# Kernel tuning notes

Hardware: AMD Instinct MI355X
Metric: run time of the kernel (lower is better)

Reference implementation:

```python
import jax, jax.numpy as jnp
import numpy as np

B, S, D_MODEL, D_ATTN = 4, 4096, 2048, 2048


def setup_inputs() -> dict:
    key = jax.random.key(0)
    ks = jax.random.split(key, 6)
    s = 0.02
    return {
        "x": jax.random.normal(ks[0], (B, S, D_MODEL), dtype=jnp.float32),
        "Wq": jax.random.normal(ks[1], (D_ATTN, D_MODEL), dtype=jnp.float32) * s,
        "Wk": jax.random.normal(ks[2], (D_ATTN, D_MODEL), dtype=jnp.float32) * s,
        "Wv": jax.random.normal(ks[3], (D_ATTN, D_MODEL), dtype=jnp.float32) * s,
        "Wo": jax.random.normal(ks[4], (D_MODEL, D_ATTN), dtype=jnp.float32) * s,
        "bo": jnp.zeros((D_MODEL,), dtype=jnp.float32),
    }


def reference(x, Wq, Wk, Wv, Wo, bo):
    # q,k,v: [B,S,d_attn] via bias-free linears (torch Linear: x @ W.T)
    q = jnp.einsum('bsd,ad->bsa', x, Wq)
    k = jnp.einsum('bsd,ad->bsa', x, Wk)
    v = jnp.einsum('bsd,ad->bsa', x, Wv)
    # logits: [B,S,S]; NOTE: source scales by sqrt(d_model), not d_attn
    scale = 1.0 / jnp.sqrt(jnp.asarray(x.shape[-1], dtype=x.dtype))
    logits = jnp.einsum('bqa,bka->bqk', q, k) * scale
    attn = jax.nn.softmax(logits, axis=-1)
    attn_out = jnp.einsum('bqk,bka->bqa', attn, v)
    return jnp.einsum('bqa,da->bqd', attn_out, Wo) + bo
```

## Files before the change

kernel.cpp:

```cpp
#include <hip/hip_runtime.h>
#include <hip/hip_bf16.h>


#define S_ 4096
#define DM_ 2048
#define DA_ 2048
#define NB_ 4

typedef __attribute__((ext_vector_type(8))) short short8;
typedef __attribute__((ext_vector_type(4))) float f32x4;
typedef __attribute__((ext_vector_type(8))) unsigned short ushort8;

__device__ __forceinline__ void gload_lds16(const void* g, void* l) {
  __builtin_amdgcn_global_load_lds(
      (const __attribute__((address_space(1))) void*)g,
      (__attribute__((address_space(3))) void*)l, 16, 0, 0);
}

__device__ __forceinline__ unsigned short f2bf(float f) {
  __hip_bfloat16 h = __float2bfloat16(f);
  return __builtin_bit_cast(unsigned short, h);
}

#define STAGE_A(par, h, kt)                                                    \
  {                                                                            \
    const __hip_bfloat16* s0 = Asrc + (size_t)((h)*128) * lda + (kt)*64;       \
    gload_lds16(s0, dstA + (par)*32768 + (h)*16384);                           \
    gload_lds16(s0 + (size_t)64 * lda, dstA + (par)*32768 + (h)*16384 + 8192); \
  }
#define STAGE_B(par, h, kt)                                                    \
  {                                                                            \
    const __hip_bfloat16* s0 = Bsrc + (size_t)((h)*128) * ldb + (kt)*64;       \
    gload_lds16(s0, dstB + (par)*32768 + (h)*16384);                           \
    gload_lds16(s0 + (size_t)64 * ldb, dstB + (par)*32768 + (h)*16384 + 8192); \
  }
#define LDA_FRAG(par, mi, i, kk) \
  (*(const short8*)(ldsAr + (par)*32768 + ((mi)*2 + (i)) * 2048 + (kk)*1024))
#define LDB_FRAG(par, j, kk) \
  (*(const short8*)(ldsBr + (par)*32768 + (j)*2048 + (kk)*1024))

#define MFMA_ON(mi, AF)                                                     \
  __builtin_amdgcn_s_setprio(1);                                            \
  _Pragma("unroll") for (int i = 0; i < 2; ++i)                             \
      _Pragma("unroll") for (int j = 0; j < 4; ++j)                         \
          _Pragma("unroll") for (int kk = 0; kk < 2; ++kk)                  \
              acc[(mi)*2 + i][j] = __builtin_amdgcn_mfma_f32_16x16x32_bf16( \
                  AF[i][kk], Bf[j][kk], acc[(mi)*2 + i][j], 0, 0, 0);       \
  __builtin_amdgcn_s_setprio(0);

#define PHASE_SYNC_PRE                               \
  __builtin_amdgcn_s_barrier();                      \
  asm volatile("s_waitcnt lgkmcnt(0)" ::: "memory"); \
  __builtin_amdgcn_sched_barrier(0);

template <int PAR>
__device__ __forceinline__ void tile_body(
    int t, int NT, const __hip_bfloat16* __restrict__ Asrc,
    const __hip_bfloat16* __restrict__ Bsrc, int lda, int ldb, char* dstA,
    char* dstB, const char* ldsAr, const char* ldsBr, f32x4 (&acc)[8][4]) {
  const int tn = min(t + 1, NT - 1);
  const int tf = min(t + 2, NT - 1);
  short8 Bf[4][2], Af[2][2];

#pragma unroll
  for (int j = 0; j < 4; ++j)
#pragma unroll
    for (int kk = 0; kk < 2; ++kk) Bf[j][kk] = LDB_FRAG(PAR, j, kk);
#pragma unroll
  for (int i = 0; i < 2; ++i)
#pragma unroll
    for (int kk = 0; kk < 2; ++kk) Af[i][kk] = LDA_FRAG(PAR, 0, i, kk);
  STAGE_A(PAR ^ 1, 0, tn);
  PHASE_SYNC_PRE
  MFMA_ON(0, Af)
  __builtin_amdgcn_s_barrier();

#pragma unroll
  for (int i = 0; i < 2; ++i)
#pragma unroll
    for (int kk = 0; kk < 2; ++kk) Af[i][kk] = LDA_FRAG(PAR, 1, i, kk);
  STAGE_A(PAR ^ 1, 1, tn);
  PHASE_SYNC_PRE
  MFMA_ON(1, Af)
  __builtin_amdgcn_s_barrier();

#pragma unroll
  for (int i = 0; i < 2; ++i)
#pragma unroll
    for (int kk = 0; kk < 2; ++kk) Af[i][kk] = LDA_FRAG(PAR, 2, i, kk);
  STAGE_B(PAR, 0, tf);
  PHASE_SYNC_PRE
  MFMA_ON(2, Af)
  __builtin_amdgcn_s_barrier();

#pragma unroll
  for (int i = 0; i < 2; ++i)
#pragma unroll
    for (int kk = 0; kk < 2; ++kk) Af[i][kk] = LDA_FRAG(PAR, 3, i, kk);
  STAGE_B(PAR, 1, tf);
  PHASE_SYNC_PRE
  MFMA_ON(3, Af)
  asm volatile("s_waitcnt vmcnt(4)" ::: "memory");
  __builtin_amdgcn_s_barrier();
  __builtin_amdgcn_sched_barrier(0);
}

template <int EPI>
__device__ __forceinline__ void gemm8_body(
    int wgin, int nwg, const __hip_bfloat16* __restrict__ A,
    const __hip_bfloat16* __restrict__ Bm, void* __restrict__ Cv,
    const float* __restrict__ bias, float* __restrict__ aux, int N, int K,
    int lda, int ldb, int ldc, float scale, long strideA, long strideB,
    long strideC) {
  __shared__ alignas(16) char lds[131072];
  const int tid = threadIdx.x;
  const int lane = tid & 63;
  const int w = tid >> 6;
  const int wr = w >> 2, wc = w & 3;

  int wg = (wgin & 7) * (nwg >> 3) + (wgin >> 3);
  const int nbn = N >> 8;
  const int nstx = nbn >> 2;
  const int st = wg >> 4;
  const int bm = (st / nstx) * 4 + ((wg >> 2) & 3);
  const int bn = (st % nstx) * 4 + (wg & 3);

  A += (long)blockIdx.y * strideA;
  Bm += (long)blockIdx.y * strideB;

  const int R = ((w >> 1) << 4) + (lane >> 2);
  const int Cc = ((w & 1) << 5) + (((lane & 3) << 3) ^ ((lane & 32) >> 1));
  const __hip_bfloat16* Asrc = A + (size_t)(bm * 256 + R) * lda + Cc;
  const __hip_bfloat16* Bsrc = Bm + (size_t)(bn * 256 + R) * ldb + Cc;
  char* dstA = lds + w * 1024 + lane * 16;
  char* dstB = dstA + 65536;

  const int fr = lane & 15;
  const int fk2 = (lane >> 4) << 4;
  const int rby = fr * 64 + (fk2 ^ ((fr & 8) << 2));
  const char* ldsAr = lds + wr * 16384 + rby;
  const char* ldsBr = lds + 65536 + (wc >> 1) * 16384 + (wc & 1) * 8192 + rby;

  const int NT = K >> 6;
  f32x4 acc[8][4] = {};

  STAGE_A(0, 0, 0)
  STAGE_A(0, 1, 0)
  STAGE_B(0, 0, 0)
  STAGE_B(0, 1, 0)
  STAGE_B(1, 0, 1)
  STAGE_B(1, 1, 1)
  asm volatile("s_waitcnt vmcnt(4)" ::: "memory");
  __builtin_amdgcn_s_barrier();
  __builtin_amdgcn_sched_barrier(0);

  for (int t = 0; t < NT; t += 2) {
    tile_body<0>(t, NT, Asrc, Bsrc, lda, ldb, dstA, dstB, ldsAr, ldsBr, acc);
    tile_body<1>(t + 1, NT, Asrc, Bsrc, lda, ldb, dstA, dstB, ldsAr, ldsBr,
                 acc);
  }
  asm volatile("s_waitcnt vmcnt(0)" ::: "memory");

  float* Cf = (float*)Cv;
  __hip_bfloat16* Cb = (__hip_bfloat16*)Cv;
  const size_t cbase = (size_t)blockIdx.y * (size_t)strideC;
  const int r0 = bm * 256 + wr * 128 + ((lane >> 4) << 2);
  const int c0 = bn * 256 + wc * 64 + fr;

  if (EPI == 3) {
    __syncthreads();
    float* rpart = (float*)lds;
#pragma unroll
    for (int mi = 0; mi < 4; ++mi) {
      float pr[8] = {};
#pragma unroll
      for (int i = 0; i < 2; ++i)
#pragma unroll
        for (int j = 0; j < 4; ++j) {
          const int row = r0 + mi * 32 + i * 16;
          const int col = c0 + j * 16;
#pragma unroll
          for (int r = 0; r < 4; ++r) {
            const float p = __expf(acc[mi * 2 + i][j][r] * scale);
            Cb[cbase + (size_t)(row + r) * ldc + col] = __float2bfloat16(p);
            pr[i * 4 + r] += p;
          }
        }
#pragma unroll
      for (int k = 0; k < 8; ++k) {
#pragma unroll
        for (int m = 1; m <= 8; m <<= 1) pr[k] += __shfl_xor(pr[k], m);
      }
      if (fr == 0) {
#pragma unroll
        for (int i = 0; i < 2; ++i)
#pragma unroll
          for (int r = 0; r < 4; ++r)
            rpart[wc * 256 + wr * 128 + mi * 32 + i * 16 +
                  ((lane >> 4) << 2) + r] = pr[i * 4 + r];
      }
    }
    __syncthreads();
    if (tid < 256) {
      const float s = rpart[tid] + rpart[256 + tid] + rpart[512 + tid] +
                      rpart[768 + tid];
      aux[(size_t)blockIdx.y * 65536 + (size_t)bn * 4096 + bm * 256 + tid] = s;
    }
    return;
  }

#pragma unroll
  for (int mi = 0; mi < 4; ++mi)
#pragma unroll
    for (int i = 0; i < 2; ++i) {
      float rsv[4];
      if (EPI == 4) {
#pragma unroll
        for (int r = 0; r < 4; ++r)
          rsv[r] = aux[(size_t)blockIdx.y * 4096 + r0 + mi * 32 + i * 16 + r];
      }
#pragma unroll
      for (int j = 0; j < 4; ++j) {
        const int row = r0 + mi * 32 + i * 16;
        const int col = c0 + j * 16;
#pragma unroll
        for (int r = 0; r < 4; ++r) {
          const float v = acc[mi * 2 + i][j][r];
          if (EPI == 0)
            Cb[cbase + (size_t)(row + r) * ldc + col] = __float2bfloat16(v);
          else if (EPI == 2)
            Cf[cbase + (size_t)(row + r) * ldc + col] = v + bias[col];
          else
            Cf[cbase + (size_t)(row + r) * ldc + col] = v * rsv[r] + bias[col];
        }
      }
    }
}

#define GEMM_WRAP(NAME, EPI)                                                   \
  __global__ __launch_bounds__(512, 1) void NAME(                              \
      const __hip_bfloat16* __restrict__ A,                                    \
      const __hip_bfloat16* __restrict__ Bm, void* __restrict__ Cv,            \
      const float* __restrict__ bias, float* __restrict__ aux, int N, int K,   \
      int lda, int ldb, int ldc, float scale, long strideA, long strideB,      \
      long strideC) {                                                          \
    gemm8_body<EPI>(blockIdx.x, gridDim.x, A, Bm, Cv, bias, aux, N, K, lda,    \
                    ldb, ldc, scale, strideA, strideB, strideC);               \
  }
GEMM_WRAP(g_small, 0)
GEMM_WRAP(g_qkt, 3)
GEMM_WRAP(g_pv, 4)

__global__ __launch_bounds__(512, 1) void g_xgvot(
    const __hip_bfloat16* __restrict__ Xb, const __hip_bfloat16* __restrict__ Gt,
    __hip_bfloat16* __restrict__ xG, const __hip_bfloat16* __restrict__ Wvo,
    __hip_bfloat16* __restrict__ VOt) {
  const int b = blockIdx.x;
  const __hip_bfloat16 *Ap, *Bp;
  __hip_bfloat16* Cp;
  int wg, nwg, N, ldc;
  if (b < 512) {
    Ap = Xb; Bp = Gt; Cp = xG;
    wg = b; nwg = 512; N = 2048; ldc = 2048;
  } else {
    const int vb = b - 512;
    const int y = vb >> 7;
    Ap = Wvo; Bp = Xb + (size_t)y * S_ * DM_; Cp = VOt + (size_t)y * DA_ * S_;
    wg = vb & 127; nwg = 128; N = 4096; ldc = 4096;
  }
  gemm8_body<0>(wg, nwg, Ap, Bp, Cp, nullptr, nullptr, N, 2048, 2048, 2048,
                ldc, 1.f, 0, 0, 0);
}

__global__ __launch_bounds__(256) void rs_inv(const float* __restrict__ PS,
                                              float* __restrict__ RSI) {
  const int t = blockIdx.x * 256 + threadIdx.x;
  const int y = t >> 12;
  const int row = t & 4095;
  float s = 0.f;
#pragma unroll
  for (int cb = 0; cb < 16; ++cb) s += PS[(size_t)y * 65536 + cb * 4096 + row];
  RSI[t] = 1.0f / s;
}

__device__ __forceinline__ void tcast64(const float* __restrict__ src,
                                        __hip_bfloat16* __restrict__ dst,
                                        int tile) {
  __shared__ __hip_bfloat16 lt[64][65];
  const int ti = tile >> 5;
  const int tj = tile & 31;
  const int t = threadIdx.x;
  const int r = t >> 4;
  const int c4 = (t & 15) * 4;
#pragma unroll
  for (int rr = 0; rr < 4; ++rr) {
    const int row = ti * 64 + rr * 16 + r;
    const f32x4 v = *(const f32x4*)(src + (size_t)row * 2048 + tj * 64 + c4);
#pragma unroll
    for (int k = 0; k < 4; ++k)
      lt[c4 + k][rr * 16 + r] = __float2bfloat16(v[k]);
  }
  __syncthreads();
  const int a = t >> 2;
  const int b16 = (t & 3) * 16;
  ushort8* dp = (ushort8*)(dst + (size_t)(tj * 64 + a) * 2048 + ti * 64 + b16);
  const unsigned short* lp = (const unsigned short*)&lt[a][b16];
  ushort8 o0, o1;
#pragma unroll
  for (int k = 0; k < 8; ++k) {
    o0[k] = lp[k];
    o1[k] = lp[8 + k];
  }
  dp[0] = o0;
  dp[1] = o1;
}

__global__ __launch_bounds__(256) void cast_all(
    const float* __restrict__ x, const float* __restrict__ wq,
    const float* __restrict__ wk, const float* __restrict__ wv,
    const float* __restrict__ wo, __hip_bfloat16* __restrict__ xb,
    __hip_bfloat16* __restrict__ wqt, __hip_bfloat16* __restrict__ wkt,
    __hip_bfloat16* __restrict__ wvt, __hip_bfloat16* __restrict__ wob) {
  const int b = blockIdx.x;
  if (b >= 18432) {
    if (b < 19456) tcast64(wq, wqt, b - 18432);
    else if (b < 20480) tcast64(wk, wkt, b - 19456);
    else tcast64(wv, wvt, b - 20480);
    return;
  }
  const float* src;
  __hip_bfloat16* dst;
  long base;
  if (b < 16384) {
    src = x; dst = xb; base = (long)b;
  } else {
    src = wo; dst = wob; base = (long)(b - 16384);
  }
  const long i = (base * 256 + threadIdx.x) * 8;
  const f32x4 a = *(const f32x4*)(src + i);
  const f32x4 c = *(const f32x4*)(src + i + 4);
  ushort8 o;
#pragma unroll
  for (int j = 0; j < 4; ++j) o[j] = f2bf(a[j]);
#pragma unroll
  for (int j = 0; j < 4; ++j) o[4 + j] = f2bf(c[j]);
  *(ushort8*)(dst + i) = o;
}

extern "C" void kernel_launch(void* const* d_in, const int* in_sizes, int n_in,
                              void* d_out, int out_size, void* d_ws,
                              size_t ws_size, hipStream_t stream) {
  (void)in_sizes; (void)n_in; (void)out_size; (void)ws_size;
  const float* x = (const float*)d_in[0];
  const float* Wq = (const float*)d_in[1];
  const float* Wk = (const float*)d_in[2];
  const float* Wv = (const float*)d_in[3];
  const float* Wo = (const float*)d_in[4];
  const float* bo = (const float*)d_in[5];
  float* out = (float*)d_out;

  const long MB = 1ll << 20;
  char* ws = (char*)d_ws;
  __hip_bfloat16* Xb  = (__hip_bfloat16*)(ws);
  __hip_bfloat16* xG  = (__hip_bfloat16*)(ws + 64 * MB);
  __hip_bfloat16* VOt = (__hip_bfloat16*)(ws + 128 * MB);
  __hip_bfloat16* WkT = (__hip_bfloat16*)(ws + 192 * MB);
  __hip_bfloat16* Wob = (__hip_bfloat16*)(ws + 200 * MB);
  __hip_bfloat16* WqT = (__hip_bfloat16*)(ws + 208 * MB);
  __hip_bfloat16* WvT = (__hip_bfloat16*)(ws + 216 * MB);
  __hip_bfloat16* Gt  = (__hip_bfloat16*)(ws + 224 * MB);
  __hip_bfloat16* Wvo = (__hip_bfloat16*)(ws + 232 * MB);
  char* LgP           = ws + 240 * MB;
  float* PS           = (float*)(ws + 368 * MB);
  float* RSI          = (float*)(ws + 369 * MB);

  const long WSTRIDE = 8 * MB / 2;

  cast_all<<<dim3(21504), dim3(256), 0, stream>>>(x, Wq, Wk, Wv, Wo, Xb, WqT,
                                                  WkT, WvT, Wob);

  g_small<<<dim3(64, 2), dim3(512), 0, stream>>>(
      WkT, WqT, Gt, nullptr, nullptr, 2048, 2048, 2048, 2048, 2048, 1.f,
      WSTRIDE, WSTRIDE, WSTRIDE);
  g_xgvot<<<dim3(1024, 1), dim3(512), 0, stream>>>(Xb, Gt, xG, Wvo, VOt);

  const float scale = 0.022097086912079608f;
  g_qkt<<<dim3(256, NB_), dim3(512), 0, stream>>>(
      xG, Xb, LgP, nullptr, PS, 4096, 2048, 2048, 2048, 4096, scale,
      (long)S_ * DA_, (long)S_ * DM_, (long)S_ * S_);
  rs_inv<<<dim3(64), dim3(256), 0, stream>>>(PS, RSI);
  g_pv<<<dim3(128, NB_), dim3(512), 0, stream>>>(
      (const __hip_bfloat16*)LgP, VOt, out, bo, RSI, 2048, 4096, 4096, 4096,
      2048, 1.f, (long)S_ * S_, (long)DA_ * S_, (long)S_ * DM_);
}
```

Measured before the change: 788.7 us.

## Fuse row-sum inversion into PV epilogue and overlap x cast with small GEMM

Removes the rs_inv kernel by having each PV GEMM block sum the partial row sums for its row tile, invert them, and share them through LDS for the epilogue. Moves the fp32-to-bf16 cast of x out of the weight-cast kernel and into extra blocks of the Wk·Wq GEMM launch, so the cast runs alongside that low-occupancy GEMM. This cuts kernel launches and serial gaps. In exchange, the PV blocks do some redundant partial-sum reads and an extra LDS barrier.

Result: no change. 780.8 us (-1.0%).

```diff
diff --git a/kernel.cpp b/kernel.cpp
--- a/kernel.cpp
+++ b/kernel.cpp
@@ -128,6 +128,15 @@
   A += (long)blockIdx.y * strideA;
   Bm += (long)blockIdx.y * strideB;
 
+  float myrsi = 0.f;
+  if (EPI == 4 && tid < 256) {
+    float s = 0.f;
+#pragma unroll
+    for (int cb = 0; cb < 16; ++cb)
+      s += aux[(size_t)blockIdx.y * 65536 + cb * 4096 + bm * 256 + tid];
+    myrsi = 1.0f / s;
+  }
+
   const int R = ((w >> 1) << 4) + (lane >> 2);
   const int Cc = ((w & 1) << 5) + (((lane & 3) << 3) ^ ((lane & 32) >> 1));
   const __hip_bfloat16* Asrc = A + (size_t)(bm * 256 + R) * lda + Cc;
@@ -209,32 +218,46 @@
     return;
   }
 
+  if (EPI == 4) {
+    __syncthreads();
+    float* ldsf = (float*)lds;
+    if (tid < 256) ldsf[tid] = myrsi;
+    __syncthreads();
+#pragma unroll
+    for (int mi = 0; mi < 4; ++mi)
+#pragma unroll
+      for (int i = 0; i < 2; ++i) {
+        float rsv[4];
+#pragma unroll
+        for (int r = 0; r < 4; ++r)
+          rsv[r] =
+              ldsf[wr * 128 + mi * 32 + i * 16 + ((lane >> 4) << 2) + r];
+#pragma unroll
+        for (int j = 0; j < 4; ++j) {
+          const int row = r0 + mi * 32 + i * 16;
+          const int col = c0 + j * 16;
+#pragma unroll
+          for (int r = 0; r < 4; ++r)
+            Cf[cbase + (size_t)(row + r) * ldc + col] =
+                acc[mi * 2 + i][j][r] * rsv[r] + bias[col];
+        }
+      }
+    return;
+  }
+
 #pragma unroll
   for (int mi = 0; mi < 4; ++mi)
 #pragma unroll
-    for (int i = 0; i < 2; ++i) {
-      float rsv[4];
-      if (EPI == 4) {
-#pragma unroll
-        for (int r = 0; r < 4; ++r)
-          rsv[r] = aux[(size_t)blockIdx.y * 4096 + r0 + mi * 32 + i * 16 + r];
-      }
+    for (int i = 0; i < 2; ++i)
 #pragma unroll
       for (int j = 0; j < 4; ++j) {
         const int row = r0 + mi * 32 + i * 16;
         const int col = c0 + j * 16;
 #pragma unroll
-        for (int r = 0; r < 4; ++r) {
-          const float v = acc[mi * 2 + i][j][r];
-          if (EPI == 0)
-            Cb[cbase + (size_t)(row + r) * ldc + col] = __float2bfloat16(v);
-          else if (EPI == 2)
-            Cf[cbase + (size_t)(row + r) * ldc + col] = v + bias[col];
-          else
-            Cf[cbase + (size_t)(row + r) * ldc + col] = v * rsv[r] + bias[col];
-        }
+        for (int r = 0; r < 4; ++r)
+          Cb[cbase + (size_t)(row + r) * ldc + col] =
+              __float2bfloat16(acc[mi * 2 + i][j][r]);
       }
-    }
 }
 
 #define GEMM_WRAP(NAME, EPI)                                                   \
@@ -247,9 +270,33 @@
     gemm8_body<EPI>(blockIdx.x, gridDim.x, A, Bm, Cv, bias, aux, N, K, lda,    \
                     ldb, ldc, scale, strideA, strideB, strideC);               \
   }
-GEMM_WRAP(g_small, 0)
 GEMM_WRAP(g_qkt, 3)
 GEMM_WRAP(g_pv, 4)
+
+__global__ __launch_bounds__(512, 1) void g_small_x(
+    const __hip_bfloat16* __restrict__ WA, const __hip_bfloat16* __restrict__ WB,
+    __hip_bfloat16* __restrict__ WC, long wstride,
+    const float* __restrict__ x, __hip_bfloat16* __restrict__ xb) {
+  const int b = blockIdx.x;
+  if (b < 64) {
+    gemm8_body<0>(b, 64, WA, WB, WC, nullptr, nullptr, 2048, 2048, 2048, 2048,
+                  2048, 1.f, wstride, wstride, wstride);
+    return;
+  }
+  const long ci = (long)blockIdx.y * 2048 + (b - 64);
+  const long base = ci * 8192 + (long)threadIdx.x * 16;
+#pragma unroll
+  for (int h = 0; h < 2; ++h) {
+    const f32x4 a = *(const f32x4*)(x + base + h * 8);
+    const f32x4 c = *(const f32x4*)(x + base + h * 8 + 4);
+    ushort8 o;
+#pragma unroll
+    for (int j = 0; j < 4; ++j) o[j] = f2bf(a[j]);
+#pragma unroll
+    for (int j = 0; j < 4; ++j) o[4 + j] = f2bf(c[j]);
+    *(ushort8*)(xb + base + h * 8) = o;
+  }
+}
 
 __global__ __launch_bounds__(512, 1) void g_xgvot(
     const __hip_bfloat16* __restrict__ Xb, const __hip_bfloat16* __restrict__ Gt,
@@ -272,17 +319,6 @@
                 ldc, 1.f, 0, 0, 0);
 }
 
-__global__ __launch_bounds__(256) void rs_inv(const float* __restrict__ PS,
-                                              float* __restrict__ RSI) {
-  const int t = blockIdx.x * 256 + threadIdx.x;
-  const int y = t >> 12;
-  const int row = t & 4095;
-  float s = 0.f;
-#pragma unroll
-  for (int cb = 0; cb < 16; ++cb) s += PS[(size_t)y * 65536 + cb * 4096 + row];
-  RSI[t] = 1.0f / s;
-}
-
 __device__ __forceinline__ void tcast64(const float* __restrict__ src,
                                         __hip_bfloat16* __restrict__ dst,
                                         int tile) {
@@ -315,36 +351,24 @@
   dp[1] = o1;
 }
 
-__global__ __launch_bounds__(256) void cast_all(
-    const float* __restrict__ x, const float* __restrict__ wq,
-    const float* __restrict__ wk, const float* __restrict__ wv,
-    const float* __restrict__ wo, __hip_bfloat16* __restrict__ xb,
+__global__ __launch_bounds__(256) void cast_w(
+    const float* __restrict__ wq, const float* __restrict__ wk,
+    const float* __restrict__ wv, const float* __restrict__ wo,
     __hip_bfloat16* __restrict__ wqt, __hip_bfloat16* __restrict__ wkt,
     __hip_bfloat16* __restrict__ wvt, __hip_bfloat16* __restrict__ wob) {
   const int b = blockIdx.x;
-  if (b >= 18432) {
-    if (b < 19456) tcast64(wq, wqt, b - 18432);
-    else if (b < 20480) tcast64(wk, wkt, b - 19456);
-    else tcast64(wv, wvt, b - 20480);
-    return;
-  }
-  const float* src;
-  __hip_bfloat16* dst;
-  long base;
-  if (b < 16384) {
-    src = x; dst = xb; base = (long)b;
-  } else {
-    src = wo; dst = wob; base = (long)(b - 16384);
-  }
-  const long i = (base * 256 + threadIdx.x) * 8;
-  const f32x4 a = *(const f32x4*)(src + i);
-  const f32x4 c = *(const f32x4*)(src + i + 4);
+  if (b < 1024) { tcast64(wq, wqt, b); return; }
+  if (b < 2048) { tcast64(wk, wkt, b - 1024); return; }
+  if (b < 3072) { tcast64(wv, wvt, b - 2048); return; }
+  const long i = ((long)(b - 3072) * 256 + threadIdx.x) * 8;
+  const f32x4 a = *(const f32x4*)(wo + i);
+  const f32x4 c = *(const f32x4*)(wo + i + 4);
   ushort8 o;
 #pragma unroll
   for (int j = 0; j < 4; ++j) o[j] = f2bf(a[j]);
 #pragma unroll
   for (int j = 0; j < 4; ++j) o[4 + j] = f2bf(c[j]);
-  *(ushort8*)(dst + i) = o;
+  *(ushort8*)(wob + i) = o;
 }
 
 extern "C" void kernel_launch(void* const* d_in, const int* in_sizes, int n_in,
@@ -372,24 +396,20 @@
   __hip_bfloat16* Wvo = (__hip_bfloat16*)(ws + 232 * MB);
   char* LgP           = ws + 240 * MB;
   float* PS           = (float*)(ws + 368 * MB);
-  float* RSI          = (float*)(ws + 369 * MB);
 
   const long WSTRIDE = 8 * MB / 2;
 
-  cast_all<<<dim3(21504), dim3(256), 0, stream>>>(x, Wq, Wk, Wv, Wo, Xb, WqT,
-                                                  WkT, WvT, Wob);
-
-  g_small<<<dim3(64, 2), dim3(512), 0, stream>>>(
-      WkT, WqT, Gt, nullptr, nullptr, 2048, 2048, 2048, 2048, 2048, 1.f,
-      WSTRIDE, WSTRIDE, WSTRIDE);
+  cast_w<<<dim3(5120), dim3(256), 0, stream>>>(Wq, Wk, Wv, Wo, WqT, WkT, WvT,
+                                               Wob);
+  g_small_x<<<dim3(2112, 2), dim3(512), 0, stream>>>(WkT, WqT, Gt, WSTRIDE, x,
+                                                     Xb);
   g_xgvot<<<dim3(1024, 1), dim3(512), 0, stream>>>(Xb, Gt, xG, Wvo, VOt);
 
   const float scale = 0.022097086912079608f;
   g_qkt<<<dim3(256, NB_), dim3(512), 0, stream>>>(
       xG, Xb, LgP, nullptr, PS, 4096, 2048, 2048, 2048, 4096, scale,
       (long)S_ * DA_, (long)S_ * DM_, (long)S_ * S_);
-  rs_inv<<<dim3(64), dim3(256), 0, stream>>>(PS, RSI);
   g_pv<<<dim3(128, NB_), dim3(512), 0, stream>>>(
-      (const __hip_bfloat16*)LgP, VOt, out, bo, RSI, 2048, 4096, 4096, 4096,
+      (const __hip_bfloat16*)LgP, VOt, out, bo, PS, 2048, 4096, 4096, 4096,
       2048, 1.f, (long)S_ * S_, (long)DA_ * S_, (long)S_ * DM_);
 }
```
